# Performance work log

Hardware: AMD Instinct MI355X
Metric: run time of the kernel (lower is better)

## Reference

```python
import jax, jax.numpy as jnp
import numpy as np

NEG_INF = -1e9  # finite large-negative for the additive causal mask
N, H, S, SKV, K, V = 4, 16, 2048, 2048, 128, 128


def setup_inputs() -> dict:
    key = jax.random.key(0)
    k1, k2, k3, k4 = jax.random.split(key, 4)
    seqs = jax.random.normal(k1, (N, H, S, K), dtype=jnp.float32)
    keys = jax.random.normal(k2, (N, H, SKV, K), dtype=jnp.float32)
    values = jax.random.normal(k3, (N, H, SKV, V), dtype=jnp.float32)
    # boolean keep-mask; force first key position valid so no row is fully masked
    kpm = jax.random.randint(k4, (N, SKV), 0, 2) > 0
    kpm = kpm.at[:, 0].set(True)
    # causal additive attention mask, shape (S, S_kv)
    causal = jnp.tril(jnp.ones((S, SKV), dtype=bool))
    attn_mask = jnp.where(causal, 0.0, NEG_INF).astype(jnp.float32)
    return {"seqs": seqs, "keys": keys, "values": values,
            "key_padding_mask": kpm, "attn_mask": attn_mask}


def reference(seqs, keys, values, key_padding_mask, attn_mask):
    # attn_weights: [N,H,S,S_kv]
    scale = seqs.shape[-1] ** -0.5
    w = jnp.einsum('bhsk,bhtk->bhst', seqs, keys) * scale
    w = w + attn_mask  # broadcast (S,S_kv) over (N,H)
    w = jnp.where(key_padding_mask[:, None, None, :], w, -jnp.inf)
    # softmax computed in fp32, then cast back to input dtype (matches torch)
    p = jax.nn.softmax(w.astype(jnp.float32), axis=-1).astype(seqs.dtype)
    attn = jnp.einsum('bhst,bhtv->bhsv', p, values)
    return attn
```

## Files before the change

### kernel.cpp

```cpp
#include <hip/hip_runtime.h>

#define S_Q 2048
#define S_KV 2048
#define D_K 128
#define NH 64
#define QSCALE 0.12751494907890272f

typedef __attribute__((ext_vector_type(8))) short s16x8;
typedef __attribute__((ext_vector_type(16))) float f32x16;

__device__ __attribute__((aligned(16))) unsigned short g_Kb[(size_t)NH * S_KV * D_K];
__device__ __attribute__((aligned(16))) unsigned short g_Vt[(size_t)NH * D_K * S_KV];

__device__ inline unsigned short f2bf(float f) {
  unsigned int u = __float_as_uint(f);
  u += 0x7FFFu + ((u >> 16) & 1u);
  return (unsigned short)(u >> 16);
}

__device__ inline void plane32_swap(unsigned& a, unsigned& b) {
#if __has_builtin(__builtin_amdgcn_permlane32_swap)
  typedef unsigned __attribute__((ext_vector_type(2))) u32x2;
  u32x2 r = __builtin_amdgcn_permlane32_swap(a, b, false, false);
  a = r.x; b = r.y;
#else
  asm volatile("v_permlane32_swap_b32 %0, %1" : "+v"(a), "+v"(b));
#endif
}

__global__ __launch_bounds__(256) void prep_k_kernel(const float* __restrict__ K) {
  size_t g = (size_t)blockIdx.x * 256 + threadIdx.x;
  const float* src = K + g * 8;
  float4 x = *(const float4*)src;
  float4 y = *(const float4*)(src + 4);
  union { uint4 q; unsigned short u[8]; } t;
  t.u[0] = f2bf(x.x); t.u[1] = f2bf(x.y); t.u[2] = f2bf(x.z); t.u[3] = f2bf(x.w);
  t.u[4] = f2bf(y.x); t.u[5] = f2bf(y.y); t.u[6] = f2bf(y.z); t.u[7] = f2bf(y.w);
  ((uint4*)g_Kb)[g] = t.q;
}

__global__ __launch_bounds__(256) void prep_v_kernel(const float* __restrict__ V) {
  __shared__ float tile_f[64][33];
  int bid = blockIdx.x;
  int bh = bid >> 7;
  int rem = bid & 127;
  int t0 = (rem >> 2) << 6;
  int v0 = (rem & 3) << 5;
  int c = threadIdx.x & 31;
  int r8 = threadIdx.x >> 5;
#pragma unroll
  for (int i = 0; i < 8; i++) {
    int r = r8 + i * 8;
    tile_f[r][c] = V[((size_t)(bh * S_KV + t0 + r)) * D_K + v0 + c];
  }
  __syncthreads();
  int vv = threadIdx.x >> 3;
  int jc = threadIdx.x & 7;
  union { uint4 q; unsigned short u[8]; } t;
#pragma unroll
  for (int u8 = 0; u8 < 8; u8++) t.u[u8] = f2bf(tile_f[jc * 8 + u8][vv]);
  *(uint4*)&g_Vt[((size_t)(bh * D_K + v0 + vv)) * S_KV + t0 + jc * 8] = t.q;
}

__global__ __launch_bounds__(256, 2) void attn_kernel(const float* __restrict__ Q,
                                                      const int* __restrict__ kpm,
                                                      float* __restrict__ out) {
  __shared__ unsigned short sK[2][32 * 136];
  __shared__ unsigned short sV[2][128 * 40];
  __shared__ unsigned sMask[64];

  const int bx = blockIdx.x;
  const int bh = ((bx & 7) << 3) | ((bx >> 3) & 7);
  int qp = bx >> 6;
  int qi = (qp & 4) ? ((qp & 8) ? qp - 8 : qp - 4) : ((qp & 8) ? 19 - qp : 15 - qp);
  const int q0 = qi << 7;
  const int tid = threadIdx.x;
  const int w = tid >> 6;
  const int ln = tid & 31;
  const int h = (tid >> 5) & 1;
  const int h8 = h * 8;
  const int qw = q0 + w * 32;
  const int qln = qw + ln;
  const int b = bh >> 4;

  {
    int base = w * 512;
#pragma unroll
    for (int rr = 0; rr < 8; rr++) {
      int idx = base + rr * 64 + (tid & 63);
      unsigned long long bal = __ballot(kpm[b * S_KV + idx] != 0);
      if ((tid & 63) == 0) {
        sMask[(base >> 5) + rr * 2] = (unsigned)bal;
        sMask[(base >> 5) + rr * 2 + 1] = (unsigned)(bal >> 32);
      }
    }
  }

  s16x8 qf[8];
  {
    const float* qrow = Q + ((size_t)(bh * S_Q + qln)) * D_K + h8;
#pragma unroll
    for (int kc = 0; kc < 8; kc++) {
      float4 x = *(const float4*)(qrow + kc * 16);
      float4 y = *(const float4*)(qrow + kc * 16 + 4);
      union { s16x8 v; unsigned short u[8]; } t;
      t.u[0] = f2bf(x.x * QSCALE); t.u[1] = f2bf(x.y * QSCALE);
      t.u[2] = f2bf(x.z * QSCALE); t.u[3] = f2bf(x.w * QSCALE);
      t.u[4] = f2bf(y.x * QSCALE); t.u[5] = f2bf(y.y * QSCALE);
      t.u[6] = f2bf(y.z * QSCALE); t.u[7] = f2bf(y.w * QSCALE);
      qf[kc] = t.v;
    }
  }

  const int id0 = tid, id1 = 256 + tid;
  const int kr0r = id0 >> 4, kr0c = (id0 & 15) * 8;
  const int kr1r = id1 >> 4, kr1c = (id1 & 15) * 8;
  const int vr0r = id0 >> 2, vr0c = (id0 & 3) * 8;
  const int vr1r = id1 >> 2, vr1c = (id1 & 3) * 8;
  uint4 rk0, rk1, rv0, rv1;
  auto load_tile = [&](int t0) {
    rk0 = *(const uint4*)&g_Kb[((size_t)(bh * S_KV + t0 + kr0r)) * D_K + kr0c];
    rk1 = *(const uint4*)&g_Kb[((size_t)(bh * S_KV + t0 + kr1r)) * D_K + kr1c];
    rv0 = *(const uint4*)&g_Vt[((size_t)(bh * D_K + vr0r)) * S_KV + t0 + vr0c];
    rv1 = *(const uint4*)&g_Vt[((size_t)(bh * D_K + vr1r)) * S_KV + t0 + vr1c];
  };
  auto store_tile = [&](int buf) {
    *(uint4*)&sK[buf][kr0r * 136 + kr0c] = rk0;
    *(uint4*)&sK[buf][kr1r * 136 + kr1c] = rk1;
    *(uint4*)&sV[buf][vr0r * 40 + vr0c] = rv0;
    *(uint4*)&sV[buf][vr1r * 40 + vr1c] = rv1;
  };

  f32x16 o[4] = {f32x16{}, f32x16{}, f32x16{}, f32x16{}};
  float lsum = 0.0f;

  const int nT = qi * 4 + 4;
  load_tile(0);
  store_tile(0);
  load_tile(32);
  __syncthreads();

  for (int i = 0; i < nT; i++) {
    const int cur = i & 1;
    if (i + 1 < nT) {
      store_tile(1 - cur);
      if (i + 2 < nT) load_tile((i + 2) * 32);
    }
    const int t0 = i * 32;
    if (t0 <= qw + 31) {
      const unsigned km = sMask[i];
      f32x16 sa = {};
#pragma unroll
      for (int kc = 0; kc < 8; kc++) {
        s16x8 kb = *(const s16x8*)&sK[cur][ln * 136 + kc * 16 + h8];
        sa = __builtin_amdgcn_mfma_f32_32x32x16_bf16(kb, qf[kc], sa, 0, 0, 0);
      }
      int thr = qln - t0;
      unsigned causal = (thr >= 31) ? 0xFFFFFFFFu : ((thr < 0) ? 0u : ((2u << thr) - 1u));
      unsigned pmh = (km & causal) >> (h * 4);
      float p[16];
#pragma unroll
      for (int r = 0; r < 16; r++) {
        const int tb = (r & 3) + 8 * (r >> 2);
        float e = __builtin_amdgcn_exp2f(sa[r]);
        float bitf = (float)((pmh >> tb) & 1u);
        p[r] = e * bitf;
        lsum += p[r];
      }
      unsigned d[8];
#pragma unroll
      for (int m = 0; m < 4; m++) {
        d[2 * m] = __builtin_amdgcn_perm(__float_as_uint(p[4 * m + 1]),
                                         __float_as_uint(p[4 * m + 0]), 0x07060302u);
        d[2 * m + 1] = __builtin_amdgcn_perm(__float_as_uint(p[4 * m + 3]),
                                             __float_as_uint(p[4 * m + 2]), 0x07060302u);
      }
      plane32_swap(d[0], d[2]); plane32_swap(d[1], d[3]);
      plane32_swap(d[4], d[6]); plane32_swap(d[5], d[7]);
      union { unsigned u[4]; s16x8 v; } pu0, pu1;
      pu0.u[0] = d[0]; pu0.u[1] = d[1]; pu0.u[2] = d[2]; pu0.u[3] = d[3];
      pu1.u[0] = d[4]; pu1.u[1] = d[5]; pu1.u[2] = d[6]; pu1.u[3] = d[7];
#pragma unroll
      for (int vt = 0; vt < 4; vt++) {
        s16x8 va = *(const s16x8*)&sV[cur][(vt * 32 + ln) * 40 + h8];
        s16x8 vb = *(const s16x8*)&sV[cur][(vt * 32 + ln) * 40 + 16 + h8];
        o[vt] = __builtin_amdgcn_mfma_f32_32x32x16_bf16(va, pu0.v, o[vt], 0, 0, 0);
        o[vt] = __builtin_amdgcn_mfma_f32_32x32x16_bf16(vb, pu1.v, o[vt], 0, 0, 0);
      }
    }
    __syncthreads();
  }

  float ltot = lsum + __shfl_xor(lsum, 32, 64);
  float invl = 1.0f / ltot;
  size_t orow = ((size_t)(bh * S_Q + qln)) * D_K;
#pragma unroll
  for (int vt = 0; vt < 4; vt++) {
#pragma unroll
    for (int qd = 0; qd < 4; qd++) {
      float4 vv;
      vv.x = o[vt][4 * qd + 0] * invl;
      vv.y = o[vt][4 * qd + 1] * invl;
      vv.z = o[vt][4 * qd + 2] * invl;
      vv.w = o[vt][4 * qd + 3] * invl;
      *(float4*)&out[orow + vt * 32 + qd * 8 + 4 * h] = vv;
    }
  }
}

extern "C" void kernel_launch(void* const* d_in, const int* in_sizes, int n_in,
                              void* d_out, int out_size, void* d_ws, size_t ws_size,
                              hipStream_t stream) {
  const float* Q = (const float*)d_in[0];
  const float* K = (const float*)d_in[1];
  const float* V = (const float*)d_in[2];
  const int* kpm = (const int*)d_in[3];
  float* out = (float*)d_out;
  hipLaunchKernelGGL(prep_k_kernel, dim3(8192), dim3(256), 0, stream, K);
  hipLaunchKernelGGL(prep_v_kernel, dim3(8192), dim3(256), 0, stream, V);
  hipLaunchKernelGGL(attn_kernel, dim3(1024), dim3(256), 0, stream, Q, kpm, out);
}
```

Baseline: 323.4 us.

## Pair causal query tiles per block, shrink blocks, merge prep kernels, MFMA rowsum

Merges the K and V bf16 prep kernels into one launch. The attention kernel now uses 128-thread blocks that each process two 64-row query tiles (pair and 31-pair), so every block does the same causal work. The softmax denominator is computed with an extra MFMA against a ones vector instead of a scalar running sum, and the mask multiply becomes a select. This trades a smaller block and two extra MFMAs per tile for balanced work and fewer launches, but each block now loads K/V tiles with more instructions per thread.

Measured after the change: 648.0 us. +100.3%, slower.

```diff
diff --git a/kernel.cpp b/kernel.cpp
--- a/kernel.cpp
+++ b/kernel.cpp
@@ -28,41 +28,43 @@
 #endif
 }
 
-__global__ __launch_bounds__(256) void prep_k_kernel(const float* __restrict__ K) {
-  size_t g = (size_t)blockIdx.x * 256 + threadIdx.x;
-  const float* src = K + g * 8;
-  float4 x = *(const float4*)src;
-  float4 y = *(const float4*)(src + 4);
-  union { uint4 q; unsigned short u[8]; } t;
-  t.u[0] = f2bf(x.x); t.u[1] = f2bf(x.y); t.u[2] = f2bf(x.z); t.u[3] = f2bf(x.w);
-  t.u[4] = f2bf(y.x); t.u[5] = f2bf(y.y); t.u[6] = f2bf(y.z); t.u[7] = f2bf(y.w);
-  ((uint4*)g_Kb)[g] = t.q;
-}
-
-__global__ __launch_bounds__(256) void prep_v_kernel(const float* __restrict__ V) {
-  __shared__ float tile_f[64][33];
+__global__ __launch_bounds__(256) void prep_kernel(const float* __restrict__ K,
+                                                   const float* __restrict__ V) {
   int bid = blockIdx.x;
-  int bh = bid >> 7;
-  int rem = bid & 127;
-  int t0 = (rem >> 2) << 6;
-  int v0 = (rem & 3) << 5;
-  int c = threadIdx.x & 31;
-  int r8 = threadIdx.x >> 5;
-#pragma unroll
-  for (int i = 0; i < 8; i++) {
-    int r = r8 + i * 8;
-    tile_f[r][c] = V[((size_t)(bh * S_KV + t0 + r)) * D_K + v0 + c];
-  }
-  __syncthreads();
-  int vv = threadIdx.x >> 3;
-  int jc = threadIdx.x & 7;
-  union { uint4 q; unsigned short u[8]; } t;
-#pragma unroll
-  for (int u8 = 0; u8 < 8; u8++) t.u[u8] = f2bf(tile_f[jc * 8 + u8][vv]);
-  *(uint4*)&g_Vt[((size_t)(bh * D_K + v0 + vv)) * S_KV + t0 + jc * 8] = t.q;
-}
-
-__global__ __launch_bounds__(256, 2) void attn_kernel(const float* __restrict__ Q,
+  if (bid < 8192) {
+    size_t g = (size_t)bid * 256 + threadIdx.x;
+    const float* src = K + g * 8;
+    float4 x = *(const float4*)src;
+    float4 y = *(const float4*)(src + 4);
+    union { uint4 q; unsigned short u[8]; } t;
+    t.u[0] = f2bf(x.x); t.u[1] = f2bf(x.y); t.u[2] = f2bf(x.z); t.u[3] = f2bf(x.w);
+    t.u[4] = f2bf(y.x); t.u[5] = f2bf(y.y); t.u[6] = f2bf(y.z); t.u[7] = f2bf(y.w);
+    ((uint4*)g_Kb)[g] = t.q;
+  } else {
+    __shared__ float tile_f[64][33];
+    bid -= 8192;
+    int bh = bid >> 7;
+    int rem = bid & 127;
+    int t0 = (rem >> 2) << 6;
+    int v0 = (rem & 3) << 5;
+    int c = threadIdx.x & 31;
+    int r8 = threadIdx.x >> 5;
+#pragma unroll
+    for (int i = 0; i < 8; i++) {
+      int r = r8 + i * 8;
+      tile_f[r][c] = V[((size_t)(bh * S_KV + t0 + r)) * D_K + v0 + c];
+    }
+    __syncthreads();
+    int vv = threadIdx.x >> 3;
+    int jc = threadIdx.x & 7;
+    union { uint4 q; unsigned short u[8]; } t;
+#pragma unroll
+    for (int u8 = 0; u8 < 8; u8++) t.u[u8] = f2bf(tile_f[jc * 8 + u8][vv]);
+    *(uint4*)&g_Vt[((size_t)(bh * D_K + v0 + vv)) * S_KV + t0 + jc * 8] = t.q;
+  }
+}
+
+__global__ __launch_bounds__(128, 2) void attn_kernel(const float* __restrict__ Q,
                                                       const int* __restrict__ kpm,
                                                       float* __restrict__ out) {
   __shared__ unsigned short sK[2][32 * 136];
@@ -71,139 +73,150 @@
 
   const int bx = blockIdx.x;
   const int bh = ((bx & 7) << 3) | ((bx >> 3) & 7);
-  int qp = bx >> 6;
-  int qi = (qp & 4) ? ((qp & 8) ? qp - 8 : qp - 4) : ((qp & 8) ? 19 - qp : 15 - qp);
-  const int q0 = qi << 7;
+  const int pair = bx >> 6;
   const int tid = threadIdx.x;
   const int w = tid >> 6;
   const int ln = tid & 31;
   const int h = (tid >> 5) & 1;
   const int h8 = h * 8;
-  const int qw = q0 + w * 32;
-  const int qln = qw + ln;
   const int b = bh >> 4;
 
-  {
-    int base = w * 512;
-#pragma unroll
-    for (int rr = 0; rr < 8; rr++) {
-      int idx = base + rr * 64 + (tid & 63);
-      unsigned long long bal = __ballot(kpm[b * S_KV + idx] != 0);
-      if ((tid & 63) == 0) {
-        sMask[(base >> 5) + rr * 2] = (unsigned)bal;
-        sMask[(base >> 5) + rr * 2 + 1] = (unsigned)(bal >> 32);
-      }
-    }
-  }
-
-  s16x8 qf[8];
-  {
-    const float* qrow = Q + ((size_t)(bh * S_Q + qln)) * D_K + h8;
-#pragma unroll
-    for (int kc = 0; kc < 8; kc++) {
-      float4 x = *(const float4*)(qrow + kc * 16);
-      float4 y = *(const float4*)(qrow + kc * 16 + 4);
-      union { s16x8 v; unsigned short u[8]; } t;
-      t.u[0] = f2bf(x.x * QSCALE); t.u[1] = f2bf(x.y * QSCALE);
-      t.u[2] = f2bf(x.z * QSCALE); t.u[3] = f2bf(x.w * QSCALE);
-      t.u[4] = f2bf(y.x * QSCALE); t.u[5] = f2bf(y.y * QSCALE);
-      t.u[6] = f2bf(y.z * QSCALE); t.u[7] = f2bf(y.w * QSCALE);
-      qf[kc] = t.v;
-    }
-  }
-
-  const int id0 = tid, id1 = 256 + tid;
-  const int kr0r = id0 >> 4, kr0c = (id0 & 15) * 8;
-  const int kr1r = id1 >> 4, kr1c = (id1 & 15) * 8;
-  const int vr0r = id0 >> 2, vr0c = (id0 & 3) * 8;
-  const int vr1r = id1 >> 2, vr1c = (id1 & 3) * 8;
-  uint4 rk0, rk1, rv0, rv1;
+#pragma unroll
+  for (int rr = 0; rr < 16; rr++) {
+    int idx = w * 1024 + rr * 64 + (tid & 63);
+    unsigned long long bal = __ballot(kpm[b * S_KV + idx] != 0);
+    if ((tid & 63) == 0) {
+      sMask[w * 32 + rr * 2] = (unsigned)bal;
+      sMask[w * 32 + rr * 2 + 1] = (unsigned)(bal >> 32);
+    }
+  }
+
+  int krr[4], kcc[4], vrr[4], vcc[4];
+#pragma unroll
+  for (int j = 0; j < 4; j++) {
+    int id = tid + 128 * j;
+    krr[j] = id >> 4; kcc[j] = (id & 15) * 8;
+    vrr[j] = id >> 2; vcc[j] = (id & 3) * 8;
+  }
+  uint4 rk[4], rv[4];
   auto load_tile = [&](int t0) {
-    rk0 = *(const uint4*)&g_Kb[((size_t)(bh * S_KV + t0 + kr0r)) * D_K + kr0c];
-    rk1 = *(const uint4*)&g_Kb[((size_t)(bh * S_KV + t0 + kr1r)) * D_K + kr1c];
-    rv0 = *(const uint4*)&g_Vt[((size_t)(bh * D_K + vr0r)) * S_KV + t0 + vr0c];
-    rv1 = *(const uint4*)&g_Vt[((size_t)(bh * D_K + vr1r)) * S_KV + t0 + vr1c];
+#pragma unroll
+    for (int j = 0; j < 4; j++) {
+      rk[j] = *(const uint4*)&g_Kb[((size_t)(bh * S_KV + t0 + krr[j])) * D_K + kcc[j]];
+      rv[j] = *(const uint4*)&g_Vt[((size_t)(bh * D_K + vrr[j])) * S_KV + t0 + vcc[j]];
+    }
   };
   auto store_tile = [&](int buf) {
-    *(uint4*)&sK[buf][kr0r * 136 + kr0c] = rk0;
-    *(uint4*)&sK[buf][kr1r * 136 + kr1c] = rk1;
-    *(uint4*)&sV[buf][vr0r * 40 + vr0c] = rv0;
-    *(uint4*)&sV[buf][vr1r * 40 + vr1c] = rv1;
+#pragma unroll
+    for (int j = 0; j < 4; j++) {
+      *(uint4*)&sK[buf][krr[j] * 136 + kcc[j]] = rk[j];
+      *(uint4*)&sV[buf][vrr[j] * 40 + vcc[j]] = rv[j];
+    }
   };
 
-  f32x16 o[4] = {f32x16{}, f32x16{}, f32x16{}, f32x16{}};
-  float lsum = 0.0f;
-
-  const int nT = qi * 4 + 4;
-  load_tile(0);
-  store_tile(0);
-  load_tile(32);
-  __syncthreads();
-
-  for (int i = 0; i < nT; i++) {
-    const int cur = i & 1;
-    if (i + 1 < nT) {
-      store_tile(1 - cur);
-      if (i + 2 < nT) load_tile((i + 2) * 32);
-    }
-    const int t0 = i * 32;
-    if (t0 <= qw + 31) {
-      const unsigned km = sMask[i];
-      f32x16 sa = {};
+  s16x8 ones;
+  {
+    union { s16x8 v; unsigned short u[8]; } t;
+#pragma unroll
+    for (int j = 0; j < 8; j++) t.u[j] = 0x3F80;
+    ones = t.v;
+  }
+
+#pragma unroll 1
+  for (int phase = 0; phase < 2; phase++) {
+    const int qj = phase ? (31 - pair) : pair;
+    const int qw = qj * 64 + w * 32;
+    const int qln = qw + ln;
+
+    s16x8 qf[8];
+    {
+      const float* qrow = Q + ((size_t)(bh * S_Q + qln)) * D_K + h8;
 #pragma unroll
       for (int kc = 0; kc < 8; kc++) {
-        s16x8 kb = *(const s16x8*)&sK[cur][ln * 136 + kc * 16 + h8];
-        sa = __builtin_amdgcn_mfma_f32_32x32x16_bf16(kb, qf[kc], sa, 0, 0, 0);
-      }
-      int thr = qln - t0;
-      unsigned causal = (thr >= 31) ? 0xFFFFFFFFu : ((thr < 0) ? 0u : ((2u << thr) - 1u));
-      unsigned pmh = (km & causal) >> (h * 4);
-      float p[16];
-#pragma unroll
-      for (int r = 0; r < 16; r++) {
-        const int tb = (r & 3) + 8 * (r >> 2);
-        float e = __builtin_amdgcn_exp2f(sa[r]);
-        float bitf = (float)((pmh >> tb) & 1u);
-        p[r] = e * bitf;
-        lsum += p[r];
-      }
-      unsigned d[8];
-#pragma unroll
-      for (int m = 0; m < 4; m++) {
-        d[2 * m] = __builtin_amdgcn_perm(__float_as_uint(p[4 * m + 1]),
-                                         __float_as_uint(p[4 * m + 0]), 0x07060302u);
-        d[2 * m + 1] = __builtin_amdgcn_perm(__float_as_uint(p[4 * m + 3]),
-                                             __float_as_uint(p[4 * m + 2]), 0x07060302u);
-      }
-      plane32_swap(d[0], d[2]); plane32_swap(d[1], d[3]);
-      plane32_swap(d[4], d[6]); plane32_swap(d[5], d[7]);
-      union { unsigned u[4]; s16x8 v; } pu0, pu1;
-      pu0.u[0] = d[0]; pu0.u[1] = d[1]; pu0.u[2] = d[2]; pu0.u[3] = d[3];
-      pu1.u[0] = d[4]; pu1.u[1] = d[5]; pu1.u[2] = d[6]; pu1.u[3] = d[7];
-#pragma unroll
-      for (int vt = 0; vt < 4; vt++) {
-        s16x8 va = *(const s16x8*)&sV[cur][(vt * 32 + ln) * 40 + h8];
-        s16x8 vb = *(const s16x8*)&sV[cur][(vt * 32 + ln) * 40 + 16 + h8];
-        o[vt] = __builtin_amdgcn_mfma_f32_32x32x16_bf16(va, pu0.v, o[vt], 0, 0, 0);
-        o[vt] = __builtin_amdgcn_mfma_f32_32x32x16_bf16(vb, pu1.v, o[vt], 0, 0, 0);
-      }
-    }
+        float4 x = *(const float4*)(qrow + kc * 16);
+        float4 y = *(const float4*)(qrow + kc * 16 + 4);
+        union { s16x8 v; unsigned short u[8]; } t;
+        t.u[0] = f2bf(x.x * QSCALE); t.u[1] = f2bf(x.y * QSCALE);
+        t.u[2] = f2bf(x.z * QSCALE); t.u[3] = f2bf(x.w * QSCALE);
+        t.u[4] = f2bf(y.x * QSCALE); t.u[5] = f2bf(y.y * QSCALE);
+        t.u[6] = f2bf(y.z * QSCALE); t.u[7] = f2bf(y.w * QSCALE);
+        qf[kc] = t.v;
+      }
+    }
+
+    f32x16 o[4] = {f32x16{}, f32x16{}, f32x16{}, f32x16{}};
+    f32x16 sl = {};
+    const int nT = qj * 2 + 2;
+
+    load_tile(0);
+    store_tile(0);
+    if (nT > 1) load_tile(32);
     __syncthreads();
-  }
-
-  float ltot = lsum + __shfl_xor(lsum, 32, 64);
-  float invl = 1.0f / ltot;
-  size_t orow = ((size_t)(bh * S_Q + qln)) * D_K;
-#pragma unroll
-  for (int vt = 0; vt < 4; vt++) {
-#pragma unroll
-    for (int qd = 0; qd < 4; qd++) {
-      float4 vv;
-      vv.x = o[vt][4 * qd + 0] * invl;
-      vv.y = o[vt][4 * qd + 1] * invl;
-      vv.z = o[vt][4 * qd + 2] * invl;
-      vv.w = o[vt][4 * qd + 3] * invl;
-      *(float4*)&out[orow + vt * 32 + qd * 8 + 4 * h] = vv;
+
+    for (int i = 0; i < nT; i++) {
+      const int cur = i & 1;
+      if (i + 1 < nT) {
+        store_tile(1 - cur);
+        if (i + 2 < nT) load_tile((i + 2) * 32);
+      }
+      const int t0 = i * 32;
+      if (t0 <= qw + 31) {
+        const unsigned km = sMask[i];
+        f32x16 sa = {};
+#pragma unroll
+        for (int kc = 0; kc < 8; kc++) {
+          s16x8 kb = *(const s16x8*)&sK[cur][ln * 136 + kc * 16 + h8];
+          sa = __builtin_amdgcn_mfma_f32_32x32x16_bf16(kb, qf[kc], sa, 0, 0, 0);
+        }
+        int thr = qln - t0;
+        unsigned causal = (thr >= 31) ? 0xFFFFFFFFu : ((thr < 0) ? 0u : ((2u << thr) - 1u));
+        unsigned pmh = (km & causal) >> (h * 4);
+        float p[16];
+#pragma unroll
+        for (int r = 0; r < 16; r++) {
+          const int tb = (r & 3) + 8 * (r >> 2);
+          float e = __builtin_amdgcn_exp2f(sa[r]);
+          p[r] = ((pmh >> tb) & 1u) ? e : 0.0f;
+        }
+        unsigned d[8];
+#pragma unroll
+        for (int m = 0; m < 4; m++) {
+          d[2 * m] = __builtin_amdgcn_perm(__float_as_uint(p[4 * m + 1]),
+                                           __float_as_uint(p[4 * m + 0]), 0x07060302u);
+          d[2 * m + 1] = __builtin_amdgcn_perm(__float_as_uint(p[4 * m + 3]),
+                                               __float_as_uint(p[4 * m + 2]), 0x07060302u);
+        }
+        plane32_swap(d[0], d[2]); plane32_swap(d[1], d[3]);
+        plane32_swap(d[4], d[6]); plane32_swap(d[5], d[7]);
+        union { unsigned u[4]; s16x8 v; } pu0, pu1;
+        pu0.u[0] = d[0]; pu0.u[1] = d[1]; pu0.u[2] = d[2]; pu0.u[3] = d[3];
+        pu1.u[0] = d[4]; pu1.u[1] = d[5]; pu1.u[2] = d[6]; pu1.u[3] = d[7];
+#pragma unroll
+        for (int vt = 0; vt < 4; vt++) {
+          s16x8 va = *(const s16x8*)&sV[cur][(vt * 32 + ln) * 40 + h8];
+          s16x8 vb = *(const s16x8*)&sV[cur][(vt * 32 + ln) * 40 + 16 + h8];
+          o[vt] = __builtin_amdgcn_mfma_f32_32x32x16_bf16(va, pu0.v, o[vt], 0, 0, 0);
+          o[vt] = __builtin_amdgcn_mfma_f32_32x32x16_bf16(vb, pu1.v, o[vt], 0, 0, 0);
+        }
+        sl = __builtin_amdgcn_mfma_f32_32x32x16_bf16(ones, pu0.v, sl, 0, 0, 0);
+        sl = __builtin_amdgcn_mfma_f32_32x32x16_bf16(ones, pu1.v, sl, 0, 0, 0);
+      }
+      __syncthreads();
+    }
+
+    float invl = 1.0f / sl[0];
+    size_t orow = ((size_t)(bh * S_Q + qln)) * D_K;
+#pragma unroll
+    for (int vt = 0; vt < 4; vt++) {
+#pragma unroll
+      for (int qd = 0; qd < 4; qd++) {
+        float4 vv;
+        vv.x = o[vt][4 * qd + 0] * invl;
+        vv.y = o[vt][4 * qd + 1] * invl;
+        vv.z = o[vt][4 * qd + 2] * invl;
+        vv.w = o[vt][4 * qd + 3] * invl;
+        *(float4*)&out[orow + vt * 32 + qd * 8 + 4 * h] = vv;
+      }
     }
   }
 }
@@ -216,7 +229,6 @@
   const float* V = (const float*)d_in[2];
   const int* kpm = (const int*)d_in[3];
   float* out = (float*)d_out;
-  hipLaunchKernelGGL(prep_k_kernel, dim3(8192), dim3(256), 0, stream, K);
-  hipLaunchKernelGGL(prep_v_kernel, dim3(8192), dim3(256), 0, stream, V);
-  hipLaunchKernelGGL(attn_kernel, dim3(1024), dim3(256), 0, stream, Q, kpm, out);
-}
+  hipLaunchKernelGGL(prep_kernel, dim3(16384), dim3(256), 0, stream, K, V);
+  hipLaunchKernelGGL(attn_kernel, dim3(1024), dim3(128), 0, stream, Q, kpm, out);
+}
```

## Pre-swizzle K/V into MFMA fragment layout and drop shared-memory staging

Applied to the files above, without the earlier changes.

The prep pass now writes K and V in bf16 in a tiled layout that matches the per-lane MFMA operand order, and the K and V preparation are merged into one launch. The attention kernel then reads K/V fragments straight from global memory (through the caches) instead of double-buffering them through LDS. This removes the LDS stores and per-tile __syncthreads, and each wave runs only its own causal tile count. It also builds the padding mask per tile with a ballot instead of a shared table, and reorders query blocks to pair heavy and light rows. The cost is that fragment loads now carry global/L2 latency with no explicit prefetch, and K/V are read once per wave rather than once per block.

Result: slower. 350.9 us (+8.5%).

```diff
diff --git a/kernel.cpp b/kernel.cpp
--- a/kernel.cpp
+++ b/kernel.cpp
@@ -9,8 +9,8 @@
 typedef __attribute__((ext_vector_type(8))) short s16x8;
 typedef __attribute__((ext_vector_type(16))) float f32x16;
 
-__device__ __attribute__((aligned(16))) unsigned short g_Kb[(size_t)NH * S_KV * D_K];
-__device__ __attribute__((aligned(16))) unsigned short g_Vt[(size_t)NH * D_K * S_KV];
+__device__ __attribute__((aligned(16))) unsigned short g_KbT[(size_t)NH * 64 * 8 * 512];
+__device__ __attribute__((aligned(16))) unsigned short g_VtT[(size_t)NH * 64 * 8 * 512];
 
 __device__ inline unsigned short f2bf(float f) {
   unsigned int u = __float_as_uint(f);
@@ -28,73 +28,73 @@
 #endif
 }
 
-__global__ __launch_bounds__(256) void prep_k_kernel(const float* __restrict__ K) {
-  size_t g = (size_t)blockIdx.x * 256 + threadIdx.x;
-  const float* src = K + g * 8;
-  float4 x = *(const float4*)src;
-  float4 y = *(const float4*)(src + 4);
-  union { uint4 q; unsigned short u[8]; } t;
-  t.u[0] = f2bf(x.x); t.u[1] = f2bf(x.y); t.u[2] = f2bf(x.z); t.u[3] = f2bf(x.w);
-  t.u[4] = f2bf(y.x); t.u[5] = f2bf(y.y); t.u[6] = f2bf(y.z); t.u[7] = f2bf(y.w);
-  ((uint4*)g_Kb)[g] = t.q;
-}
-
-__global__ __launch_bounds__(256) void prep_v_kernel(const float* __restrict__ V) {
-  __shared__ float tile_f[64][33];
-  int bid = blockIdx.x;
-  int bh = bid >> 7;
-  int rem = bid & 127;
-  int t0 = (rem >> 2) << 6;
-  int v0 = (rem & 3) << 5;
-  int c = threadIdx.x & 31;
-  int r8 = threadIdx.x >> 5;
+__global__ __launch_bounds__(256) void prep_kernel(const float* __restrict__ K,
+                                                   const float* __restrict__ V) {
+  __shared__ float smem[32 * 132];
+  const int bid = blockIdx.x;
+  const int tid = threadIdx.x;
+  if (bid < 4096) {
+    const int bh = bid >> 6, tile = bid & 63;
+    unsigned short* sT = (unsigned short*)smem;
+    const float* src = K + ((size_t)(bh * S_KV + tile * 32)) * D_K + tid * 16;
+    union { uint4 q; unsigned short u[8]; } t0, t1;
+    float4 a0 = ((const float4*)src)[0], a1 = ((const float4*)src)[1];
+    float4 a2 = ((const float4*)src)[2], a3 = ((const float4*)src)[3];
+    t0.u[0] = f2bf(a0.x); t0.u[1] = f2bf(a0.y); t0.u[2] = f2bf(a0.z); t0.u[3] = f2bf(a0.w);
+    t0.u[4] = f2bf(a1.x); t0.u[5] = f2bf(a1.y); t0.u[6] = f2bf(a1.z); t0.u[7] = f2bf(a1.w);
+    t1.u[0] = f2bf(a2.x); t1.u[1] = f2bf(a2.y); t1.u[2] = f2bf(a2.z); t1.u[3] = f2bf(a2.w);
+    t1.u[4] = f2bf(a3.x); t1.u[5] = f2bf(a3.y); t1.u[6] = f2bf(a3.z); t1.u[7] = f2bf(a3.w);
+    *(uint4*)&sT[tid * 16] = t0.q;
+    *(uint4*)&sT[tid * 16 + 8] = t1.q;
+    __syncthreads();
+    const size_t obase = (size_t)bid * 4096;
 #pragma unroll
-  for (int i = 0; i < 8; i++) {
-    int r = r8 + i * 8;
-    tile_f[r][c] = V[((size_t)(bh * S_KV + t0 + r)) * D_K + v0 + c];
+    for (int rep = 0; rep < 2; rep++) {
+      int o = tid + rep * 256;
+      int kc = o >> 6, l = o & 63, ln = l & 31, h = l >> 5;
+      uint4 val = *(const uint4*)&sT[ln * 128 + kc * 16 + h * 8];
+      *(uint4*)&g_KbT[obase + (size_t)kc * 512 + l * 8] = val;
+    }
+  } else {
+    const int b2 = bid - 4096;
+    const int bh = b2 >> 6, tile = b2 & 63;
+    const float* src = V + ((size_t)(bh * S_KV + tile * 32)) * D_K + tid * 16;
+    const int tr = (tid * 16) >> 7, vc = (tid * 16) & 127;
+#pragma unroll
+    for (int j = 0; j < 4; j++)
+      *(float4*)&smem[tr * 132 + vc + 4 * j] = ((const float4*)src)[j];
+    __syncthreads();
+    const size_t obase = (size_t)b2 * 4096;
+#pragma unroll
+    for (int rep = 0; rep < 2; rep++) {
+      int o = tid + rep * 256;
+      int c8 = o >> 6, l = o & 63, ln = l & 31, h = l >> 5;
+      int vt = c8 >> 1, hh = c8 & 1;
+      union { uint4 q; unsigned short u[8]; } t;
+#pragma unroll
+      for (int j = 0; j < 8; j++)
+        t.u[j] = f2bf(smem[(hh * 16 + h * 8 + j) * 132 + vt * 32 + ln]);
+      *(uint4*)&g_VtT[obase + (size_t)c8 * 512 + l * 8] = t.q;
+    }
   }
-  __syncthreads();
-  int vv = threadIdx.x >> 3;
-  int jc = threadIdx.x & 7;
-  union { uint4 q; unsigned short u[8]; } t;
-#pragma unroll
-  for (int u8 = 0; u8 < 8; u8++) t.u[u8] = f2bf(tile_f[jc * 8 + u8][vv]);
-  *(uint4*)&g_Vt[((size_t)(bh * D_K + v0 + vv)) * S_KV + t0 + jc * 8] = t.q;
 }
 
 __global__ __launch_bounds__(256, 2) void attn_kernel(const float* __restrict__ Q,
                                                       const int* __restrict__ kpm,
                                                       float* __restrict__ out) {
-  __shared__ unsigned short sK[2][32 * 136];
-  __shared__ unsigned short sV[2][128 * 40];
-  __shared__ unsigned sMask[64];
-
   const int bx = blockIdx.x;
   const int bh = ((bx & 7) << 3) | ((bx >> 3) & 7);
-  int qp = bx >> 6;
-  int qi = (qp & 4) ? ((qp & 8) ? qp - 8 : qp - 4) : ((qp & 8) ? 19 - qp : 15 - qp);
-  const int q0 = qi << 7;
+  const int qp = bx >> 6;
+  const int qi = (qp & 1) ? (qp >> 1) : (15 - (qp >> 1));
   const int tid = threadIdx.x;
   const int w = tid >> 6;
+  const int l6 = tid & 63;
   const int ln = tid & 31;
   const int h = (tid >> 5) & 1;
   const int h8 = h * 8;
-  const int qw = q0 + w * 32;
+  const int qw = qi * 128 + w * 32;
   const int qln = qw + ln;
   const int b = bh >> 4;
-
-  {
-    int base = w * 512;
-#pragma unroll
-    for (int rr = 0; rr < 8; rr++) {
-      int idx = base + rr * 64 + (tid & 63);
-      unsigned long long bal = __ballot(kpm[b * S_KV + idx] != 0);
-      if ((tid & 63) == 0) {
-        sMask[(base >> 5) + rr * 2] = (unsigned)bal;
-        sMask[(base >> 5) + rr * 2 + 1] = (unsigned)(bal >> 32);
-      }
-    }
-  }
 
   s16x8 qf[8];
   {
@@ -112,83 +112,58 @@
     }
   }
 
-  const int id0 = tid, id1 = 256 + tid;
-  const int kr0r = id0 >> 4, kr0c = (id0 & 15) * 8;
-  const int kr1r = id1 >> 4, kr1c = (id1 & 15) * 8;
-  const int vr0r = id0 >> 2, vr0c = (id0 & 3) * 8;
-  const int vr1r = id1 >> 2, vr1c = (id1 & 3) * 8;
-  uint4 rk0, rk1, rv0, rv1;
-  auto load_tile = [&](int t0) {
-    rk0 = *(const uint4*)&g_Kb[((size_t)(bh * S_KV + t0 + kr0r)) * D_K + kr0c];
-    rk1 = *(const uint4*)&g_Kb[((size_t)(bh * S_KV + t0 + kr1r)) * D_K + kr1c];
-    rv0 = *(const uint4*)&g_Vt[((size_t)(bh * D_K + vr0r)) * S_KV + t0 + vr0c];
-    rv1 = *(const uint4*)&g_Vt[((size_t)(bh * D_K + vr1r)) * S_KV + t0 + vr1c];
-  };
-  auto store_tile = [&](int buf) {
-    *(uint4*)&sK[buf][kr0r * 136 + kr0c] = rk0;
-    *(uint4*)&sK[buf][kr1r * 136 + kr1c] = rk1;
-    *(uint4*)&sV[buf][vr0r * 40 + vr0c] = rv0;
-    *(uint4*)&sV[buf][vr1r * 40 + vr1c] = rv1;
-  };
+  const unsigned short* Kb = g_KbT + (size_t)bh * 64 * 4096 + l6 * 8;
+  const unsigned short* Vb = g_VtT + (size_t)bh * 64 * 4096 + l6 * 8;
+  const int* kpmb = kpm + b * S_KV + ln;
 
   f32x16 o[4] = {f32x16{}, f32x16{}, f32x16{}, f32x16{}};
   float lsum = 0.0f;
 
-  const int nT = qi * 4 + 4;
-  load_tile(0);
-  store_tile(0);
-  load_tile(32);
-  __syncthreads();
+  const int nI = qi * 4 + w + 1;
+  for (int i = 0; i < nI; i++) {
+    const int t0 = i * 32;
+    unsigned long long bal = __ballot(kpmb[t0] != 0);
+    const unsigned km = (unsigned)bal;
 
-  for (int i = 0; i < nT; i++) {
-    const int cur = i & 1;
-    if (i + 1 < nT) {
-      store_tile(1 - cur);
-      if (i + 2 < nT) load_tile((i + 2) * 32);
+    const unsigned short* kt = Kb + (size_t)i * 4096;
+    f32x16 sa = {};
+#pragma unroll
+    for (int kc = 0; kc < 8; kc++) {
+      s16x8 kb = *(const s16x8*)(kt + kc * 512);
+      sa = __builtin_amdgcn_mfma_f32_32x32x16_bf16(kb, qf[kc], sa, 0, 0, 0);
     }
-    const int t0 = i * 32;
-    if (t0 <= qw + 31) {
-      const unsigned km = sMask[i];
-      f32x16 sa = {};
+    int thr = qln - t0;
+    unsigned causal = (thr >= 31) ? 0xFFFFFFFFu : ((thr < 0) ? 0u : ((2u << thr) - 1u));
+    unsigned pmh = (km & causal) >> (h * 4);
+    float p[16];
 #pragma unroll
-      for (int kc = 0; kc < 8; kc++) {
-        s16x8 kb = *(const s16x8*)&sK[cur][ln * 136 + kc * 16 + h8];
-        sa = __builtin_amdgcn_mfma_f32_32x32x16_bf16(kb, qf[kc], sa, 0, 0, 0);
-      }
-      int thr = qln - t0;
-      unsigned causal = (thr >= 31) ? 0xFFFFFFFFu : ((thr < 0) ? 0u : ((2u << thr) - 1u));
-      unsigned pmh = (km & causal) >> (h * 4);
-      float p[16];
+    for (int r = 0; r < 16; r++) {
+      const int tb = (r & 3) + 8 * (r >> 2);
+      float e = __builtin_amdgcn_exp2f(sa[r]);
+      p[r] = ((pmh >> tb) & 1u) ? e : 0.0f;
+      lsum += p[r];
+    }
+    unsigned d[8];
 #pragma unroll
-      for (int r = 0; r < 16; r++) {
-        const int tb = (r & 3) + 8 * (r >> 2);
-        float e = __builtin_amdgcn_exp2f(sa[r]);
-        float bitf = (float)((pmh >> tb) & 1u);
-        p[r] = e * bitf;
-        lsum += p[r];
-      }
-      unsigned d[8];
+    for (int m = 0; m < 4; m++) {
+      d[2 * m] = __builtin_amdgcn_perm(__float_as_uint(p[4 * m + 1]),
+                                       __float_as_uint(p[4 * m + 0]), 0x07060302u);
+      d[2 * m + 1] = __builtin_amdgcn_perm(__float_as_uint(p[4 * m + 3]),
+                                           __float_as_uint(p[4 * m + 2]), 0x07060302u);
+    }
+    plane32_swap(d[0], d[2]); plane32_swap(d[1], d[3]);
+    plane32_swap(d[4], d[6]); plane32_swap(d[5], d[7]);
+    union { unsigned u[4]; s16x8 v; } pu0, pu1;
+    pu0.u[0] = d[0]; pu0.u[1] = d[1]; pu0.u[2] = d[2]; pu0.u[3] = d[3];
+    pu1.u[0] = d[4]; pu1.u[1] = d[5]; pu1.u[2] = d[6]; pu1.u[3] = d[7];
+    const unsigned short* vtp = Vb + (size_t)i * 4096;
 #pragma unroll
-      for (int m = 0; m < 4; m++) {
-        d[2 * m] = __builtin_amdgcn_perm(__float_as_uint(p[4 * m + 1]),
-                                         __float_as_uint(p[4 * m + 0]), 0x07060302u);
-        d[2 * m + 1] = __builtin_amdgcn_perm(__float_as_uint(p[4 * m + 3]),
-                                             __float_as_uint(p[4 * m + 2]), 0x07060302u);
-      }
-      plane32_swap(d[0], d[2]); plane32_swap(d[1], d[3]);
-      plane32_swap(d[4], d[6]); plane32_swap(d[5], d[7]);
-      union { unsigned u[4]; s16x8 v; } pu0, pu1;
-      pu0.u[0] = d[0]; pu0.u[1] = d[1]; pu0.u[2] = d[2]; pu0.u[3] = d[3];
-      pu1.u[0] = d[4]; pu1.u[1] = d[5]; pu1.u[2] = d[6]; pu1.u[3] = d[7];
-#pragma unroll
-      for (int vt = 0; vt < 4; vt++) {
-        s16x8 va = *(const s16x8*)&sV[cur][(vt * 32 + ln) * 40 + h8];
-        s16x8 vb = *(const s16x8*)&sV[cur][(vt * 32 + ln) * 40 + 16 + h8];
-        o[vt] = __builtin_amdgcn_mfma_f32_32x32x16_bf16(va, pu0.v, o[vt], 0, 0, 0);
-        o[vt] = __builtin_amdgcn_mfma_f32_32x32x16_bf16(vb, pu1.v, o[vt], 0, 0, 0);
-      }
+    for (int vt = 0; vt < 4; vt++) {
+      s16x8 va = *(const s16x8*)(vtp + (vt * 2) * 512);
+      s16x8 vb = *(const s16x8*)(vtp + (vt * 2 + 1) * 512);
+      o[vt] = __builtin_amdgcn_mfma_f32_32x32x16_bf16(va, pu0.v, o[vt], 0, 0, 0);
+      o[vt] = __builtin_amdgcn_mfma_f32_32x32x16_bf16(vb, pu1.v, o[vt], 0, 0, 0);
     }
-    __syncthreads();
   }
 
   float ltot = lsum + __shfl_xor(lsum, 32, 64);
@@ -216,7 +191,6 @@
   const float* V = (const float*)d_in[2];
   const int* kpm = (const int*)d_in[3];
   float* out = (float*)d_out;
-  hipLaunchKernelGGL(prep_k_kernel, dim3(8192), dim3(256), 0, stream, K);
-  hipLaunchKernelGGL(prep_v_kernel, dim3(8192), dim3(256), 0, stream, V);
+  hipLaunchKernelGGL(prep_kernel, dim3(8192), dim3(256), 0, stream, K, V);
   hipLaunchKernelGGL(attn_kernel, dim3(1024), dim3(256), 0, stream, Q, kpm, out);
 }
```
